# Performance work log

Measured on AMD Instinct MI355X. Metric: run time of the kernel, lower is better.

The kernel has to match this reference:

```python
import jax, jax.numpy as jnp
import numpy as np

B, H, LQ, LV, D = 32, 8, 256, 1024, 512


def setup_inputs() -> dict:
    key = jax.random.key(0)
    ks = jax.random.split(key, 10)
    sc = 0.02
    return {
        "queries": jax.random.normal(ks[0], (B, H, LQ, D), jnp.float32),
        "keys": jax.random.normal(ks[1], (B, LV, D), jnp.float32),
        "values": jax.random.normal(ks[2], (B, LV, D), jnp.float32),
        "W_q": sc * jax.random.normal(ks[3], (D, D), jnp.float32),
        "W_k": sc * jax.random.normal(ks[4], (D, D), jnp.float32),
        "W_v": sc * jax.random.normal(ks[5], (D, D), jnp.float32),
        "W_o": sc * jax.random.normal(ks[6], (D, D), jnp.float32),
        "W_len": sc * jax.random.normal(ks[7], (LQ, LV), jnp.float32),
        "b_len": sc * jax.random.normal(ks[8], (LQ,), jnp.float32),
        "valid_lens": jax.random.randint(ks[9], (B,), 0, LQ).astype(jnp.int32),
    }


def _multi_len_att(x, W_len, b_len):
    # x: [B, LV, D]; torch does permute(0,2,1) then Linear(LV->LQ) then
    # permute back; the identical linear is repeated per head (broadcast).
    # result per head: [B, LQ, D]
    return jnp.einsum('bld,ql->bqd', x, W_len) + b_len[None, :, None]


def reference(queries, keys, values, W_q, W_k, W_v, W_o, W_len, b_len, valid_lens):
    # queries: [B, H, LQ, D] -> W_q -> merge batch/head
    q = jnp.einsum('bhqd,ed->bhqe', queries, W_q).reshape(B * H, LQ, D)
    # keys/values: length-projection (shared across heads), then W_k/W_v
    k1 = jnp.einsum('bqd,ed->bqe', _multi_len_att(keys, W_len, b_len), W_k)   # [B, LQ, D]
    v1 = jnp.einsum('bqd,ed->bqe', _multi_len_att(values, W_len, b_len), W_v)  # [B, LQ, D]
    k = jnp.broadcast_to(k1[:, None], (B, H, LQ, D)).reshape(B * H, LQ, D)
    v = jnp.broadcast_to(v1[:, None], (B, H, LQ, D)).reshape(B * H, LQ, D)
    # scaled dot-product attention with valid-length masking
    scores = jnp.einsum('nqd,nkd->nqk', q, k) / jnp.sqrt(jnp.float32(D))  # [B*H, LQ, LQ]
    vl = jnp.repeat(valid_lens, H)                                        # [B*H]
    mask = jnp.arange(LQ)[None, None, :] < vl[:, None, None]
    scores = jnp.where(mask, scores, jnp.float32(-1e6))
    attn = jax.nn.softmax(scores, axis=-1)
    out = jnp.einsum('nqk,nkd->nqd', attn, v).reshape(B, H, LQ, D)
    return jnp.einsum('bhqd,ed->bhqe', out, W_o)
```

## Files before the change

### kernel.cpp

```cpp
#include <hip/hip_runtime.h>
#include <math.h>

#define Bc  32
#define Hc  8
#define LQc 256
#define LVc 1024
#define Dc  512

#define VMCNT0 asm volatile("s_waitcnt vmcnt(0)" ::: "memory")

typedef short bf16x8 __attribute__((ext_vector_type(8)));
typedef float f32x4  __attribute__((ext_vector_type(4)));

__device__ __forceinline__ unsigned short f2bf(float x) {
    unsigned u = __builtin_bit_cast(unsigned, x);
    u = (u + 0x7fffu + ((u >> 16) & 1u)) >> 16;
    return (unsigned short)u;
}

__device__ __forceinline__ bf16x8 pack8(float4 a, float4 b) {
    bf16x8 r;
    r[0] = (short)f2bf(a.x); r[1] = (short)f2bf(a.y);
    r[2] = (short)f2bf(a.z); r[3] = (short)f2bf(a.w);
    r[4] = (short)f2bf(b.x); r[5] = (short)f2bf(b.y);
    r[6] = (short)f2bf(b.z); r[7] = (short)f2bf(b.w);
    return r;
}

__device__ __forceinline__ void gload16(const ushort* g, ushort* l) {
    __builtin_amdgcn_global_load_lds(
        (const __attribute__((address_space(1))) unsigned*)g,
        (__attribute__((address_space(3))) unsigned*)l, 16, 0, 0);
}

__global__ __launch_bounds__(256) void prep_w(const float* __restrict__ Wq,
                                              const float* __restrict__ Wk,
                                              const float* __restrict__ Wv,
                                              const float* __restrict__ Wo,
                                              const float* __restrict__ Wl,
                                              ushort* __restrict__ wqT,
                                              ushort* __restrict__ wkT,
                                              ushort* __restrict__ wvT,
                                              ushort* __restrict__ woBf,
                                              ushort* __restrict__ wlBf) {
    const int z = blockIdx.z;
    if (z < 3) {
        __shared__ float t[32][33];
        const float* in = (z == 0) ? Wq : (z == 1) ? Wk : Wv;
        ushort* out = (z == 0) ? wqT : (z == 1) ? wkT : wvT;
        const int l0 = blockIdx.x * 32, d0 = blockIdx.y * 32;
        const int r = threadIdx.x >> 5, c = threadIdx.x & 31;
#pragma unroll
        for (int i = 0; i < 4; i++)
            t[r + 8 * i][c] = in[(size_t)(l0 + r + 8 * i) * 512 + d0 + c];
        __syncthreads();
#pragma unroll
        for (int i = 0; i < 4; i++)
            out[(size_t)(d0 + r + 8 * i) * 512 + l0 + c] = f2bf(t[c][r + 8 * i]);
    } else {
        const float* in = (z == 3) ? Wo : Wl;
        ushort* out = (z == 3) ? woBf : wlBf;
        const int i = (blockIdx.y * 16 + blockIdx.x) * 256 + threadIdx.x;
        float4 v = ((const float4*)in)[i];
        ushort4 o;
        o.x = f2bf(v.x); o.y = f2bf(v.y); o.z = f2bf(v.z); o.w = f2bf(v.w);
        ((ushort4*)out)[i] = o;
    }
}

__global__ __launch_bounds__(256) void lenproj_f32(const ushort* __restrict__ wl,
                                                   const float* __restrict__ keys,
                                                   const float* __restrict__ vals,
                                                   const float* __restrict__ bias,
                                                   ushort* __restrict__ t1k) {
    __shared__ __align__(16) ushort Wls[4096];
    __shared__ __align__(16) float  Xsf[128 * 36];

    const int z = blockIdx.z;
    const float* X = ((z < 32) ? keys : vals) + (size_t)(z & 31) * LVc * Dc;
    ushort* C = t1k + (size_t)z * LQc * Dc;

    const int bm = blockIdx.y * 128;
    const int bn = blockIdx.x * 128;
    const int tid = threadIdx.x;
    const int wave = tid >> 6, l = tid & 63;
    const int wm = (wave >> 1) * 64, wn = (wave & 1) * 64;
    const int l15 = l & 15, lh = l >> 4;

    f32x4 acc[4][4];
#pragma unroll
    for (int m = 0; m < 4; m++)
#pragma unroll
        for (int n = 0; n < 4; n++) acc[m][n] = (f32x4){0.f, 0.f, 0.f, 0.f};

    const int lrow = tid >> 3;
    const int dcol = (tid & 7) * 16;

    for (int l0 = 0; l0 < LVc; l0 += 32) {
        gload16(wl + (size_t)(bm + wave * 16 + l15) * LVc + l0 + lh * 8,
                Wls + wave * 512);
        gload16(wl + (size_t)(bm + 64 + wave * 16 + l15) * LVc + l0 + lh * 8,
                Wls + (wave + 4) * 512);
        const float* xs = X + (size_t)(l0 + lrow) * Dc + bn + dcol;
        float4 xv0 = ((const float4*)xs)[0];
        float4 xv1 = ((const float4*)xs)[1];
        float4 xv2 = ((const float4*)xs)[2];
        float4 xv3 = ((const float4*)xs)[3];
        Xsf[(dcol + 0)  * 36 + lrow] = xv0.x;
        Xsf[(dcol + 1)  * 36 + lrow] = xv0.y;
        Xsf[(dcol + 2)  * 36 + lrow] = xv0.z;
        Xsf[(dcol + 3)  * 36 + lrow] = xv0.w;
        Xsf[(dcol + 4)  * 36 + lrow] = xv1.x;
        Xsf[(dcol + 5)  * 36 + lrow] = xv1.y;
        Xsf[(dcol + 6)  * 36 + lrow] = xv1.z;
        Xsf[(dcol + 7)  * 36 + lrow] = xv1.w;
        Xsf[(dcol + 8)  * 36 + lrow] = xv2.x;
        Xsf[(dcol + 9)  * 36 + lrow] = xv2.y;
        Xsf[(dcol + 10) * 36 + lrow] = xv2.z;
        Xsf[(dcol + 11) * 36 + lrow] = xv2.w;
        Xsf[(dcol + 12) * 36 + lrow] = xv3.x;
        Xsf[(dcol + 13) * 36 + lrow] = xv3.y;
        Xsf[(dcol + 14) * 36 + lrow] = xv3.z;
        Xsf[(dcol + 15) * 36 + lrow] = xv3.w;
        VMCNT0;
        __syncthreads();

        bf16x8 af[4], bfr[4];
#pragma unroll
        for (int m = 0; m < 4; m++)
            af[m] = *(const bf16x8*)&Wls[((wm >> 4) + m) * 512 + lh * 128 + l15 * 8];
#pragma unroll
        for (int n = 0; n < 4; n++) {
            const float* fb = &Xsf[(wn + n * 16 + l15) * 36 + lh * 8];
            float4 x0 = *(const float4*)fb;
            float4 x1 = *(const float4*)(fb + 4);
            bfr[n] = pack8(x0, x1);
        }
#pragma unroll
        for (int m = 0; m < 4; m++)
#pragma unroll
            for (int n = 0; n < 4; n++)
                acc[m][n] = __builtin_amdgcn_mfma_f32_16x16x32_bf16(
                    af[m], bfr[n], acc[m][n], 0, 0, 0);
        __syncthreads();
    }

#pragma unroll
    for (int m = 0; m < 4; m++)
#pragma unroll
        for (int r = 0; r < 4; r++) {
            const int row = bm + wm + m * 16 + lh * 4 + r;
            const float bv = bias[row];
#pragma unroll
            for (int n = 0; n < 4; n++) {
                const int col = bn + wn + n * 16 + l15;
                C[(size_t)row * Dc + col] = f2bf(acc[m][n][r] + bv);
            }
        }
}

template <int STORE, bool BIAS, int SWIZ>
__global__ __launch_bounds__(256) void gemm_bt(const ushort* __restrict__ A,
                                               const ushort* __restrict__ B,
                                               void* __restrict__ Cv,
                                               const float* __restrict__ bias,
                                               int M, int N, int K, float alpha,
                                               long sA, long sB, long sC,
                                               int byPerXcd) {
    __shared__ ushort As[128 * 32];
    __shared__ ushort Bs[128 * 32];
    const int z = blockIdx.z;
    A += (size_t)z * sA;
    B += (size_t)z * sB;
    float*  Cf = (float*)Cv  + (size_t)z * sC;
    ushort* Ch = (ushort*)Cv + (size_t)z * sC;

    int bm, bn;
    if constexpr (SWIZ) {
        const int bid = blockIdx.x;
        const int xcd = bid & 7, slot = bid >> 3;
        bm = (xcd * byPerXcd + (slot >> 2)) * 128;
        bn = (slot & 3) * 128;
    } else {
        bm = blockIdx.y * 128;
        bn = blockIdx.x * 128;
    }
    const int tid = threadIdx.x;
    const int wave = tid >> 6, l = tid & 63;
    const int wm = (wave >> 1) * 64, wn = (wave & 1) * 64;
    const int l15 = l & 15, lh = l >> 4;

    f32x4 acc[4][4];
#pragma unroll
    for (int m = 0; m < 4; m++)
#pragma unroll
        for (int n = 0; n < 4; n++) acc[m][n] = (f32x4){0.f, 0.f, 0.f, 0.f};

    const int srow = tid >> 2, scol = (tid & 3) * 8;
    ushort* ldsA = As + (wave * 16) * 32;
    ushort* ldsB = Bs + (wave * 16) * 32;
    const ushort* gA = A + (size_t)(bm + srow) * K + scol;
    const ushort* gB = B + (size_t)(bn + srow) * K + scol;

    for (int k0 = 0; k0 < K; k0 += 32) {
        gload16(gA + k0, ldsA);
        gload16(gA + k0 + (size_t)64 * K, ldsA + 64 * 32);
        gload16(gB + k0, ldsB);
        gload16(gB + k0 + (size_t)64 * K, ldsB + 64 * 32);
        VMCNT0;
        __syncthreads();
        bf16x8 af[4], bfr[4];
#pragma unroll
        for (int m = 0; m < 4; m++)
            af[m] = *(const bf16x8*)&As[(wm + m * 16 + l15) * 32 + lh * 8];
#pragma unroll
        for (int n = 0; n < 4; n++)
            bfr[n] = *(const bf16x8*)&Bs[(wn + n * 16 + l15) * 32 + lh * 8];
#pragma unroll
        for (int m = 0; m < 4; m++)
#pragma unroll
            for (int n = 0; n < 4; n++)
                acc[m][n] = __builtin_amdgcn_mfma_f32_16x16x32_bf16(
                    af[m], bfr[n], acc[m][n], 0, 0, 0);
        __syncthreads();
    }

    if constexpr (STORE == 2) {
#pragma unroll
        for (int m = 0; m < 4; m++) {
            const int row0 = bm + wm + m * 16 + lh * 4;
            const int bb = row0 >> 8, q = row0 & 255;
            float bv[4] = {0.f, 0.f, 0.f, 0.f};
            if constexpr (BIAS) {
#pragma unroll
                for (int r = 0; r < 4; r++) bv[r] = bias[q + r];
            }
#pragma unroll
            for (int n = 0; n < 4; n++) {
                const int col = bn + wn + n * 16 + l15;
                ushort4 o;
                o.x = f2bf(acc[m][n][0] * alpha + bv[0]);
                o.y = f2bf(acc[m][n][1] * alpha + bv[1]);
                o.z = f2bf(acc[m][n][2] * alpha + bv[2]);
                o.w = f2bf(acc[m][n][3] * alpha + bv[3]);
                *(ushort4*)&Ch[(size_t)bb * N * 256 + (size_t)col * 256 + q] = o;
            }
        }
    } else if constexpr (STORE == 1) {
#pragma unroll
        for (int m = 0; m < 4; m++)
#pragma unroll
            for (int r = 0; r < 4; r++) {
                const int row = bm + wm + m * 16 + lh * 4 + r;
                const float bv = BIAS ? bias[row & 255] : 0.f;
#pragma unroll
                for (int n = 0; n < 4; n++) {
                    const int col = bn + wn + n * 16 + l15;
                    Ch[(size_t)row * N + col] = f2bf(acc[m][n][r] * alpha + bv);
                }
            }
    } else {
#pragma unroll
        for (int m = 0; m < 4; m++)
#pragma unroll
            for (int r = 0; r < 4; r++) {
                const int row = bm + wm + m * 16 + lh * 4 + r;
                const float bv = BIAS ? bias[row & 255] : 0.f;
#pragma unroll
                for (int n = 0; n < 4; n++) {
                    const int col = bn + wn + n * 16 + l15;
                    Cf[(size_t)row * N + col] = acc[m][n][r] * alpha + bv;
                }
            }
    }
}

__global__ __launch_bounds__(256, 2) void attn_mfma(const float* __restrict__ qf,
                                                    const ushort* __restrict__ k2,
                                                    const ushort* __restrict__ v2T,
                                                    const int* __restrict__ vlen,
                                                    float* __restrict__ aout) {
    __shared__ __align__(16) ushort pool[40960];
    ushort* Ps = pool;

    const int bid = blockIdx.x;
    const int xcd = bid & 7, pos = bid >> 3;
    const int b = xcd * 4 + (pos >> 4);
    const int inner = pos & 15;
    const int h = inner >> 1, qh = inner & 1;
    const int n = b * 8 + h;
    const int q0 = qh * 128;

    const int tid = threadIdx.x, wave = tid >> 6, l = tid & 63;
    const int l15 = l & 15, lh = l >> 4;
    const int vl = vlen[b];

    const float*  qbase = qf  + ((size_t)n * LQc + q0) * Dc;
    const ushort* kbase = k2  + (size_t)b * LQc * Dc;
    const ushort* vbase = v2T + (size_t)b * LQc * Dc;

    f32x4 sacc[2][16];
#pragma unroll
    for (int m = 0; m < 2; m++)
#pragma unroll
        for (int fn = 0; fn < 16; fn++) sacc[m][fn] = (f32x4){0.f, 0.f, 0.f, 0.f};

    auto STAGE_K = [&](int bi, int k0) {
        ushort* k_ = pool + bi * 8192;
#pragma unroll
        for (int j = 0; j < 4; j++)
            gload16(kbase + (size_t)((j * 4 + wave) * 16 + l15) * Dc + k0 + lh * 8,
                    k_ + (j * 4 + wave) * 512);
    };

    STAGE_K(0, 0);
    VMCNT0;
    __syncthreads();
    for (int t = 0; t < 16; ++t) {
        const int k0 = t * 32;
        if (t < 15) STAGE_K((t + 1) & 1, k0 + 32);
        bf16x8 aq[2];
#pragma unroll
        for (int m2 = 0; m2 < 2; ++m2) {
            const float* fb = qbase + (size_t)(wave * 32 + m2 * 16 + l15) * Dc + k0 + lh * 8;
            float4 x0 = *(const float4*)fb;
            float4 x1 = *(const float4*)(fb + 4);
            aq[m2] = pack8(x0, x1);
        }
        const ushort* k_ = pool + (t & 1) * 8192;
#pragma unroll
        for (int fn = 0; fn < 16; fn++) {
            bf16x8 bk = *(const bf16x8*)&k_[fn * 512 + lh * 128 + l15 * 8];
            sacc[0][fn] = __builtin_amdgcn_mfma_f32_16x16x32_bf16(aq[0], bk, sacc[0][fn], 0, 0, 0);
            sacc[1][fn] = __builtin_amdgcn_mfma_f32_16x16x32_bf16(aq[1], bk, sacc[1][fn], 0, 0, 0);
        }
        VMCNT0;
        __syncthreads();
    }

    auto STAGE_V = [&](int bi, int it) {
        const int d0 = (it >> 3) * 128, l0 = (it & 7) * 32;
        ushort* v_ = pool + 32768 + bi * 4096;
        gload16(vbase + (size_t)(d0 + wave * 16 + l15) * LQc + l0 + lh * 8,
                v_ + wave * 512);
        gload16(vbase + (size_t)(d0 + 64 + wave * 16 + l15) * LQc + l0 + lh * 8,
                v_ + (wave + 4) * 512);
    };
    STAGE_V(0, 0);

#pragma unroll
    for (int m = 0; m < 2; m++)
#pragma unroll
        for (int r = 0; r < 4; r++) {
            float v[16];
            float rmax = -3.4e38f;
#pragma unroll
            for (int fn = 0; fn < 16; fn++) {
                const int col = fn * 16 + l15;
                float s = sacc[m][fn][r];
                v[fn] = (col < vl) ? s : -1e6f;
                rmax = fmaxf(rmax, v[fn]);
            }
            rmax = fmaxf(rmax, __shfl_xor(rmax, 1));
            rmax = fmaxf(rmax, __shfl_xor(rmax, 2));
            rmax = fmaxf(rmax, __shfl_xor(rmax, 4));
            rmax = fmaxf(rmax, __shfl_xor(rmax, 8));
            float rsum = 0.f;
#pragma unroll
            for (int fn = 0; fn < 16; fn++) {
                v[fn] = __expf(v[fn] - rmax);
                rsum += v[fn];
            }
            rsum += __shfl_xor(rsum, 1);
            rsum += __shfl_xor(rsum, 2);
            rsum += __shfl_xor(rsum, 4);
            rsum += __shfl_xor(rsum, 8);
            const float rinv = 1.0f / rsum;
            const int base = (wave * 2 + m) * 4096 + (lh * 4 + r) * 8 + (l15 & 7);
            const int chi = (l15 >> 3) * 128;
#pragma unroll
            for (int fn = 0; fn < 16; fn++)
                Ps[base + fn * 256 + chi] = f2bf(v[fn] * rinv);
        }
    VMCNT0;
    __syncthreads();

    int it = 0;
    for (int d0 = 0; d0 < Dc; d0 += 128) {
        f32x4 o[8][2];
#pragma unroll
        for (int qf2 = 0; qf2 < 8; qf2++) {
            o[qf2][0] = (f32x4){0.f, 0.f, 0.f, 0.f};
            o[qf2][1] = (f32x4){0.f, 0.f, 0.f, 0.f};
        }
        for (int l0 = 0; l0 < LQc; l0 += 32, ++it) {
            if (it < 31) STAGE_V((it + 1) & 1, it + 1);
            const ushort* v_ = pool + 32768 + (it & 1) * 4096;
            bf16x8 vb[2];
            vb[0] = *(const bf16x8*)&v_[(2 * wave + 0) * 512 + lh * 128 + l15 * 8];
            vb[1] = *(const bf16x8*)&v_[(2 * wave + 1) * 512 + lh * 128 + l15 * 8];
            const int pcol = (l0 >> 3) + lh;
#pragma unroll
            for (int qf2 = 0; qf2 < 8; qf2++) {
                bf16x8 pa = *(const bf16x8*)&Ps[qf2 * 4096 + pcol * 128 + l15 * 8];
                o[qf2][0] = __builtin_amdgcn_mfma_f32_16x16x32_bf16(pa, vb[0], o[qf2][0], 0, 0, 0);
                o[qf2][1] = __builtin_amdgcn_mfma_f32_16x16x32_bf16(pa, vb[1], o[qf2][1], 0, 0, 0);
            }
            VMCNT0;
            __syncthreads();
        }
#pragma unroll
        for (int qf2 = 0; qf2 < 8; qf2++)
#pragma unroll
            for (int r = 0; r < 4; r++) {
                const int rowl = qf2 * 16 + lh * 4 + r;
#pragma unroll
                for (int df = 0; df < 2; df++) {
                    const int col = d0 + wave * 32 + df * 16 + l15;
                    aout[((size_t)n * LQc + q0 + rowl) * Dc + col] = o[qf2][df][r];
                }
            }
    }
}

extern "C" void kernel_launch(void* const* d_in, const int* in_sizes, int n_in,
                              void* d_out, int out_size, void* d_ws, size_t ws_size,
                              hipStream_t stream) {
    const float* queries    = (const float*)d_in[0];
    const float* keys       = (const float*)d_in[1];
    const float* values     = (const float*)d_in[2];
    const float* W_q        = (const float*)d_in[3];
    const float* W_k        = (const float*)d_in[4];
    const float* W_v        = (const float*)d_in[5];
    const float* W_o        = (const float*)d_in[6];
    const float* W_len      = (const float*)d_in[7];
    const float* b_len      = (const float*)d_in[8];
    const int*   valid_lens = (const int*)d_in[9];

    char* ws = (char*)d_ws;
    const size_t MB = 1024 * 1024;
    ushort* woBf = (ushort*)(ws + 128 * MB);
    ushort* wl   = woBf + 262144;
    ushort* wqT  = wl   + 262144;
    ushort* wkT  = wqT  + 262144;
    ushort* wvT  = wkT  + 262144;
    ushort* Eq   = wvT  + 262144;
    ushort* G    = Eq   + 262144;
    ushort* t1k  = G    + 262144;
    ushort* t1v  = t1k  + 4194304;
    ushort* k2   = t1v  + 4194304;
    ushort* v2T  = k2   + 4194304;

    const float alpha_q = 0.044194173824159216f;
    dim3 blk(256);

    prep_w<<<dim3(16, 16, 5), blk, 0, stream>>>(W_q, W_k, W_v, W_o, W_len,
                                                wqT, wkT, wvT, woBf, wl);
    gemm_bt<1, false, 0><<<dim3(4, 4, 1), blk, 0, stream>>>(
        wqT, wkT, Eq, nullptr, 512, 512, 512, 1.f, 0, 0, 0, 0);
    gemm_bt<1, false, 0><<<dim3(4, 4, 1), blk, 0, stream>>>(
        woBf, wvT, G, nullptr, 512, 512, 512, 1.f, 0, 0, 0, 0);

    lenproj_f32<<<dim3(4, 2, 64), blk, 0, stream>>>(wl, keys, values, b_len, t1k);

    gemm_bt<1, false, 1><<<dim3(256), blk, 0, stream>>>(
        t1k, Eq, k2, nullptr, 8192, 512, 512, alpha_q, 0, 0, 0, 8);
    gemm_bt<2, false, 1><<<dim3(256), blk, 0, stream>>>(
        t1v, G, v2T, nullptr, 8192, 512, 512, 1.f, 0, 0, 0, 8);

    attn_mfma<<<dim3(512), blk, 0, stream>>>(queries, k2, v2T, valid_lens,
                                             (float*)d_out);
}
```

Measured before the change: 220.5 us.

## Split attention kernel work across 8 waves per block instead of 4

The attention kernel now runs 512 threads (8 waves) per block. Each wave owns 16 query rows in the QK^T phase and 16 output columns in the PV phase, where before it owned 32 rows and 32 columns. This halves the per-thread accumulator registers and staging loads, which should raise wave-level parallelism and help hide latency. In exchange, every wave re-reads the shared K and V fragments from LDS, so LDS reads grow relative to MFMA work, and the block-wide barriers now synchronize twice as many waves.

Result: no change. 223.8 us (+1.5%).

```diff
diff --git a/kernel.cpp b/kernel.cpp
--- a/kernel.cpp
+++ b/kernel.cpp
@@ -275,7 +275,7 @@
     }
 }
 
-__global__ __launch_bounds__(256, 2) void attn_mfma(const float* __restrict__ qf,
+__global__ __launch_bounds__(512, 2) void attn_mfma(const float* __restrict__ qf,
                                                     const ushort* __restrict__ k2,
                                                     const ushort* __restrict__ v2T,
                                                     const int* __restrict__ vlen,
@@ -299,18 +299,16 @@
     const ushort* kbase = k2  + (size_t)b * LQc * Dc;
     const ushort* vbase = v2T + (size_t)b * LQc * Dc;
 
-    f32x4 sacc[2][16];
-#pragma unroll
-    for (int m = 0; m < 2; m++)
-#pragma unroll
-        for (int fn = 0; fn < 16; fn++) sacc[m][fn] = (f32x4){0.f, 0.f, 0.f, 0.f};
+    f32x4 sacc[16];
+#pragma unroll
+    for (int fn = 0; fn < 16; fn++) sacc[fn] = (f32x4){0.f, 0.f, 0.f, 0.f};
 
     auto STAGE_K = [&](int bi, int k0) {
         ushort* k_ = pool + bi * 8192;
 #pragma unroll
-        for (int j = 0; j < 4; j++)
-            gload16(kbase + (size_t)((j * 4 + wave) * 16 + l15) * Dc + k0 + lh * 8,
-                    k_ + (j * 4 + wave) * 512);
+        for (int j = 0; j < 2; j++)
+            gload16(kbase + (size_t)((wave * 2 + j) * 16 + l15) * Dc + k0 + lh * 8,
+                    k_ + (wave * 2 + j) * 512);
     };
 
     STAGE_K(0, 0);
@@ -319,20 +317,15 @@
     for (int t = 0; t < 16; ++t) {
         const int k0 = t * 32;
         if (t < 15) STAGE_K((t + 1) & 1, k0 + 32);
-        bf16x8 aq[2];
-#pragma unroll
-        for (int m2 = 0; m2 < 2; ++m2) {
-            const float* fb = qbase + (size_t)(wave * 32 + m2 * 16 + l15) * Dc + k0 + lh * 8;
-            float4 x0 = *(const float4*)fb;
-            float4 x1 = *(const float4*)(fb + 4);
-            aq[m2] = pack8(x0, x1);
-        }
+        const float* fb = qbase + (size_t)(wave * 16 + l15) * Dc + k0 + lh * 8;
+        float4 x0 = *(const float4*)fb;
+        float4 x1 = *(const float4*)(fb + 4);
+        bf16x8 aq = pack8(x0, x1);
         const ushort* k_ = pool + (t & 1) * 8192;
 #pragma unroll
         for (int fn = 0; fn < 16; fn++) {
             bf16x8 bk = *(const bf16x8*)&k_[fn * 512 + lh * 128 + l15 * 8];
-            sacc[0][fn] = __builtin_amdgcn_mfma_f32_16x16x32_bf16(aq[0], bk, sacc[0][fn], 0, 0, 0);
-            sacc[1][fn] = __builtin_amdgcn_mfma_f32_16x16x32_bf16(aq[1], bk, sacc[1][fn], 0, 0, 0);
+            sacc[fn] = __builtin_amdgcn_mfma_f32_16x16x32_bf16(aq, bk, sacc[fn], 0, 0, 0);
         }
         VMCNT0;
         __syncthreads();
@@ -343,68 +336,60 @@
         ushort* v_ = pool + 32768 + bi * 4096;
         gload16(vbase + (size_t)(d0 + wave * 16 + l15) * LQc + l0 + lh * 8,
                 v_ + wave * 512);
-        gload16(vbase + (size_t)(d0 + 64 + wave * 16 + l15) * LQc + l0 + lh * 8,
-                v_ + (wave + 4) * 512);
     };
     STAGE_V(0, 0);
 
 #pragma unroll
-    for (int m = 0; m < 2; m++)
-#pragma unroll
-        for (int r = 0; r < 4; r++) {
-            float v[16];
-            float rmax = -3.4e38f;
-#pragma unroll
-            for (int fn = 0; fn < 16; fn++) {
-                const int col = fn * 16 + l15;
-                float s = sacc[m][fn][r];
-                v[fn] = (col < vl) ? s : -1e6f;
-                rmax = fmaxf(rmax, v[fn]);
-            }
-            rmax = fmaxf(rmax, __shfl_xor(rmax, 1));
-            rmax = fmaxf(rmax, __shfl_xor(rmax, 2));
-            rmax = fmaxf(rmax, __shfl_xor(rmax, 4));
-            rmax = fmaxf(rmax, __shfl_xor(rmax, 8));
-            float rsum = 0.f;
-#pragma unroll
-            for (int fn = 0; fn < 16; fn++) {
-                v[fn] = __expf(v[fn] - rmax);
-                rsum += v[fn];
-            }
-            rsum += __shfl_xor(rsum, 1);
-            rsum += __shfl_xor(rsum, 2);
-            rsum += __shfl_xor(rsum, 4);
-            rsum += __shfl_xor(rsum, 8);
-            const float rinv = 1.0f / rsum;
-            const int base = (wave * 2 + m) * 4096 + (lh * 4 + r) * 8 + (l15 & 7);
-            const int chi = (l15 >> 3) * 128;
-#pragma unroll
-            for (int fn = 0; fn < 16; fn++)
-                Ps[base + fn * 256 + chi] = f2bf(v[fn] * rinv);
-        }
+    for (int r = 0; r < 4; r++) {
+        const int rowl = wave * 16 + lh * 4 + r;
+        float v[16];
+        float rmax = -3.4e38f;
+#pragma unroll
+        for (int fn = 0; fn < 16; fn++) {
+            const int col = fn * 16 + l15;
+            float s = sacc[fn][r];
+            v[fn] = (col < vl) ? s : -1e6f;
+            rmax = fmaxf(rmax, v[fn]);
+        }
+        rmax = fmaxf(rmax, __shfl_xor(rmax, 1));
+        rmax = fmaxf(rmax, __shfl_xor(rmax, 2));
+        rmax = fmaxf(rmax, __shfl_xor(rmax, 4));
+        rmax = fmaxf(rmax, __shfl_xor(rmax, 8));
+        float rsum = 0.f;
+#pragma unroll
+        for (int fn = 0; fn < 16; fn++) {
+            v[fn] = __expf(v[fn] - rmax);
+            rsum += v[fn];
+        }
+        rsum += __shfl_xor(rsum, 1);
+        rsum += __shfl_xor(rsum, 2);
+        rsum += __shfl_xor(rsum, 4);
+        rsum += __shfl_xor(rsum, 8);
+        const float rinv = 1.0f / rsum;
+        const int base = wave * 4096 + (lh * 4 + r) * 8 + (l15 & 7);
+        const int chi = (l15 >> 3) * 128;
+#pragma unroll
+        for (int fn = 0; fn < 16; fn++)
+            Ps[base + fn * 256 + chi] = f2bf(v[fn] * rinv);
+    }
     VMCNT0;
     __syncthreads();
 
     int it = 0;
     for (int d0 = 0; d0 < Dc; d0 += 128) {
-        f32x4 o[8][2];
-#pragma unroll
-        for (int qf2 = 0; qf2 < 8; qf2++) {
-            o[qf2][0] = (f32x4){0.f, 0.f, 0.f, 0.f};
-            o[qf2][1] = (f32x4){0.f, 0.f, 0.f, 0.f};
-        }
+        f32x4 o[8];
+#pragma unroll
+        for (int qf2 = 0; qf2 < 8; qf2++) o[qf2] = (f32x4){0.f, 0.f, 0.f, 0.f};
+
         for (int l0 = 0; l0 < LQc; l0 += 32, ++it) {
             if (it < 31) STAGE_V((it + 1) & 1, it + 1);
             const ushort* v_ = pool + 32768 + (it & 1) * 4096;
-            bf16x8 vb[2];
-            vb[0] = *(const bf16x8*)&v_[(2 * wave + 0) * 512 + lh * 128 + l15 * 8];
-            vb[1] = *(const bf16x8*)&v_[(2 * wave + 1) * 512 + lh * 128 + l15 * 8];
+            bf16x8 vb = *(const bf16x8*)&v_[wave * 512 + lh * 128 + l15 * 8];
             const int pcol = (l0 >> 3) + lh;
 #pragma unroll
             for (int qf2 = 0; qf2 < 8; qf2++) {
                 bf16x8 pa = *(const bf16x8*)&Ps[qf2 * 4096 + pcol * 128 + l15 * 8];
-                o[qf2][0] = __builtin_amdgcn_mfma_f32_16x16x32_bf16(pa, vb[0], o[qf2][0], 0, 0, 0);
-                o[qf2][1] = __builtin_amdgcn_mfma_f32_16x16x32_bf16(pa, vb[1], o[qf2][1], 0, 0, 0);
+                o[qf2] = __builtin_amdgcn_mfma_f32_16x16x32_bf16(pa, vb, o[qf2], 0, 0, 0);
             }
             VMCNT0;
             __syncthreads();
@@ -414,11 +399,8 @@
 #pragma unroll
             for (int r = 0; r < 4; r++) {
                 const int rowl = qf2 * 16 + lh * 4 + r;
-#pragma unroll
-                for (int df = 0; df < 2; df++) {
-                    const int col = d0 + wave * 32 + df * 16 + l15;
-                    aout[((size_t)n * LQc + q0 + rowl) * Dc + col] = o[qf2][df][r];
-                }
+                const int col = d0 + wave * 16 + l15;
+                aout[((size_t)n * LQc + q0 + rowl) * Dc + col] = o[qf2][r];
             }
     }
 }
@@ -468,6 +450,6 @@
     gemm_bt<2, false, 1><<<dim3(256), blk, 0, stream>>>(
         t1v, G, v2T, nullptr, 8192, 512, 512, 1.f, 0, 0, 0, 8);
 
-    attn_mfma<<<dim3(512), blk, 0, stream>>>(queries, k2, v2T, valid_lens,
-                                             (float*)d_out);
-}
+    attn_mfma<<<dim3(512), dim3(512), 0, stream>>>(queries, k2, v2T, valid_lens,
+                                                   (float*)d_out);
+}
```
